# Kernel optimization log

Measured on AMD Instinct MI355X. Metric: run time of the kernel, lower is better.

Reference implementation:

```python
import jax, jax.numpy as jnp
import numpy as np

N_SRC = 50000   # e.g. users
N_DST = 50000   # e.g. items
N = N_SRC + N_DST
E = 1_600_000   # edges (avg degree ~16)
D = 64          # in_size == out_size


def _xavier(key, shape):
    # xavier_uniform for Linear(weight shape [out, in])
    fan_out, fan_in = shape
    limit = jnp.sqrt(6.0 / (fan_in + fan_out)).astype(jnp.float32)
    return jax.random.uniform(key, shape, jnp.float32, -limit, limit)


def setup_inputs() -> dict:
    key = jax.random.key(0)
    ks = jax.random.split(key, 8)
    return {
        "src_embedding": jax.random.normal(ks[0], (N_SRC, D), jnp.float32),
        "dst_embedding": jax.random.normal(ks[1], (N_DST, D), jnp.float32),
        "norm": jax.random.uniform(ks[2], (E, 1), jnp.float32),
        "W1": _xavier(ks[3], (D, D)),
        "b1": jnp.zeros((D,), jnp.float32),
        "W2": _xavier(ks[4], (D, D)),
        "b2": jnp.zeros((D,), jnp.float32),
        "edges_src": jax.random.randint(ks[5], (E,), 0, N, dtype=jnp.int32),
        "edges_dst": jax.random.randint(ks[6], (E,), 0, N, dtype=jnp.int32),
    }


def reference(src_embedding, dst_embedding, norm, W1, b1, W2, b2,
              edges_src, edges_dst):
    # concat user/item node tables: [N, D]
    x = jnp.concatenate([src_embedding, dst_embedding], axis=0)
    xs = x[edges_src]                      # [E, D] gather (edge source nodes)
    xd = x[edges_dst]                      # [E, D] gather (edge dest nodes)
    # msgs = W1(x_src) + W2(x_src * x_dst), per edge
    msgs = (jnp.einsum('ed,od->eo', xs, W1) + b1
            + jnp.einsum('ed,od->eo', xs * xd, W2) + b2)   # [E, D]
    msgs = norm * msgs                     # per-edge scalar normalization
    # copy_e + sum: scatter-sum messages onto destination nodes
    h = jax.ops.segment_sum(msgs, edges_dst, num_segments=N)  # [N, D]
    # LeakyReLU(0.2); dropout is identity in eval / p=0
    return jnp.where(h > 0, h, 0.2 * h)
```

## Files before the change

### kernel.cpp

```cpp
#include <hip/hip_runtime.h>
#include <hip/hip_bf16.h>


#define CHUNK 4096
#define NBMAX 1024
#define BCAP  2304

typedef __attribute__((ext_vector_type(8))) short short8v;
typedef __attribute__((ext_vector_type(4))) float f32x4;
union U4S8 { uint4 u; short8v s; };

__device__ __forceinline__ unsigned int f2bf(float f) {
    unsigned int u = __float_as_uint(f);
    u += 0x7fffu + ((u >> 16) & 1u);
    return u >> 16;
}
__device__ __forceinline__ unsigned int pkbf(float lo, float hi) {
    return (f2bf(hi) << 16) | f2bf(lo);
}

__global__ __launch_bounds__(256) void prep_init_kernel(
    const float* __restrict__ srcEmb, const float* __restrict__ dstEmb,
    unsigned int* __restrict__ xbf, int* __restrict__ gcur,
    int Ntot, int n_src, int NB)
{
    int i = blockIdx.x * 256 + threadIdx.x;
    if (i < NB) gcur[i] = i * BCAP;
    if (i >= Ntot * 32) return;
    int n = i >> 5, w = i & 31;
    const float* row = (n < n_src) ? srcEmb + (size_t)n * 64
                                   : dstEmb + (size_t)(n - n_src) * 64;
    xbf[i] = (f2bf(row[w + 32]) << 16) | f2bf(row[w]);
}

__global__ __launch_bounds__(1024) void part_scatter_kernel(
    const int* __restrict__ es, const int* __restrict__ ed,
    const float* __restrict__ norm, int* __restrict__ gcur,
    uint2* __restrict__ epk, int E, int NB)
{
    __shared__ int   bcnt[NBMAX];
    __shared__ int   lstart[NBMAX];
    __shared__ int   gbase[NBMAX];
    __shared__ int   sc[NBMAX];
    __shared__ uint2 sorted[CHUNK];

    int t  = threadIdx.x;
    int e0 = blockIdx.x * CHUNK;

    bcnt[t] = 0;
    __syncthreads();

    int dreg[4];
    #pragma unroll
    for (int k = 0; k < 4; ++k) {
        int e = e0 + t + k * 1024;
        dreg[k] = (e < E) ? ed[e] : -1;
        if (dreg[k] >= 0) atomicAdd(&bcnt[dreg[k] >> 7], 1);
    }
    __syncthreads();

    int c = (t < NB) ? bcnt[t] : 0;
    sc[t] = c;
    __syncthreads();
    for (int off = 1; off < NBMAX; off <<= 1) {
        int x = 0;
        if (t >= off) x = sc[t - off];
        __syncthreads();
        if (t >= off) sc[t] += x;
        __syncthreads();
    }
    int ex = sc[t] - c;
    lstart[t] = ex;
    bcnt[t]   = ex;
    if (c > 0) gbase[t] = atomicAdd(&gcur[t], c);
    __syncthreads();

    #pragma unroll
    for (int k = 0; k < 4; ++k) {
        int e = e0 + t + k * 1024;
        if (dreg[k] >= 0) {
            unsigned int q = (unsigned int)(norm[e] * 32767.f + 0.5f);
            if (q > 32767u) q = 32767u;
            int lp = atomicAdd(&bcnt[dreg[k] >> 7], 1);
            uint2 r; r.x = (unsigned int)es[e];
            r.y = ((unsigned int)dreg[k] << 15) | q;
            sorted[lp] = r;
        }
    }
    __syncthreads();

    int total = E - e0; if (total > CHUNK) total = CHUNK;
    for (int i = t; i < total; i += 1024) {
        uint2 r = sorted[i];
        int b = (int)(r.y >> 22);
        int gpos = gbase[b] + (i - lstart[b]);
        if (gpos < (b + 1) * BCAP)
            epk[gpos] = r;
    }
}

__global__ __launch_bounds__(512) void accum_fused_kernel(
    const unsigned int* __restrict__ xbf,
    const int* __restrict__ gcur, const uint2* __restrict__ epk,
    unsigned int* __restrict__ Acat, float* __restrict__ cnt, int Ntot)
{
    __shared__ uint2 srt[BCAP];
    __shared__ int   bh[128];
    __shared__ int   sc[128];
    __shared__ int   offs[129];

    int b = blockIdx.x, t = threadIdx.x;
    int base  = b * BCAP;
    int total = gcur[b] - base;
    if (total > BCAP) total = BCAP;

    if (t < 128) bh[t] = 0;
    __syncthreads();
    for (int i = t; i < total; i += 512)
        atomicAdd(&bh[(epk[base + i].y >> 15) & 127], 1);
    __syncthreads();

    int v = 0;
    if (t < 128) { v = bh[t]; sc[t] = v; }
    __syncthreads();
    for (int off = 1; off < 128; off <<= 1) {
        int x = 0;
        if (t < 128 && t >= off) x = sc[t - off];
        __syncthreads();
        if (t < 128 && t >= off) sc[t] += x;
        __syncthreads();
    }
    if (t < 128) {
        int ex = sc[t] - v;
        offs[t] = ex;
        if (t == 127) offs[128] = sc[127];
        bh[t] = ex;
    }
    __syncthreads();

    for (int i = t; i < total; i += 512) {
        uint2 r = epk[base + i];
        int pos = atomicAdd(&bh[(r.y >> 15) & 127], 1);
        srt[pos] = r;
    }
    __syncthreads();

    int lane = t & 63;
    int wv   = t >> 6;
    int sl   = lane & 7;
    int g    = lane >> 3;

    for (int li = 0; li < 16; ++li) {
        int loc = wv + li * 8;
        int n   = b * 128 + loc;
        int s0  = offs[loc];
        int s1  = offs[loc + 1];

        float ax0 = 0.f, ax1 = 0.f, ax2 = 0.f, ax3 = 0.f;
        float ay0 = 0.f, ay1 = 0.f, ay2 = 0.f, ay3 = 0.f;
        float c = 0.f;

        for (int bs2 = s0; bs2 < s1; bs2 += 64) {
            int m = s1 - bs2; if (m > 64) m = 64;
            unsigned int px = 0u, py = 0u;
            if (lane < m) { uint2 pk = srt[bs2 + lane]; px = pk.x; py = pk.y; }
            for (int k = 0; k < m; k += 16) {
                unsigned int sx0 = __shfl(px, k + g);
                unsigned int sy0 = __shfl(py, k + g);
                unsigned int sx1 = __shfl(px, k + 8 + g);
                unsigned int sy1 = __shfl(py, k + 8 + g);
                uint4 u0 = *(const uint4*)(xbf + (size_t)sx0 * 32 + 4 * sl);
                uint4 u1 = *(const uint4*)(xbf + (size_t)sx1 * 32 + 4 * sl);
                float w0 = (float)(sy0 & 0x7fffu) * (1.f / 32767.f);
                float w1 = (float)(sy1 & 0x7fffu) * (1.f / 32767.f);
                ax0 = fmaf(w0, __uint_as_float(u0.x << 16), ax0);
                ax1 = fmaf(w0, __uint_as_float(u0.y << 16), ax1);
                ax2 = fmaf(w0, __uint_as_float(u0.z << 16), ax2);
                ax3 = fmaf(w0, __uint_as_float(u0.w << 16), ax3);
                ay0 = fmaf(w0, __uint_as_float(u0.x & 0xffff0000u), ay0);
                ay1 = fmaf(w0, __uint_as_float(u0.y & 0xffff0000u), ay1);
                ay2 = fmaf(w0, __uint_as_float(u0.z & 0xffff0000u), ay2);
                ay3 = fmaf(w0, __uint_as_float(u0.w & 0xffff0000u), ay3);
                c += w0;
                ax0 = fmaf(w1, __uint_as_float(u1.x << 16), ax0);
                ax1 = fmaf(w1, __uint_as_float(u1.y << 16), ax1);
                ax2 = fmaf(w1, __uint_as_float(u1.z << 16), ax2);
                ax3 = fmaf(w1, __uint_as_float(u1.w << 16), ax3);
                ay0 = fmaf(w1, __uint_as_float(u1.x & 0xffff0000u), ay0);
                ay1 = fmaf(w1, __uint_as_float(u1.y & 0xffff0000u), ay1);
                ay2 = fmaf(w1, __uint_as_float(u1.z & 0xffff0000u), ay2);
                ay3 = fmaf(w1, __uint_as_float(u1.w & 0xffff0000u), ay3);
                c += w1;
            }
        }

        #pragma unroll
        for (int off = 8; off < 64; off <<= 1) {
            ax0 += __shfl_xor(ax0, off); ax1 += __shfl_xor(ax1, off);
            ax2 += __shfl_xor(ax2, off); ax3 += __shfl_xor(ax3, off);
            ay0 += __shfl_xor(ay0, off); ay1 += __shfl_xor(ay1, off);
            ay2 += __shfl_xor(ay2, off); ay3 += __shfl_xor(ay3, off);
            c   += __shfl_xor(c,   off);
        }

        if (g == 0 && n < Ntot) {
            uint4 xv = *(const uint4*)(xbf + (size_t)n * 32 + 4 * sl);
            float xl0 = __uint_as_float(xv.x << 16);
            float xl1 = __uint_as_float(xv.y << 16);
            float xl2 = __uint_as_float(xv.z << 16);
            float xl3 = __uint_as_float(xv.w << 16);
            float xh0 = __uint_as_float(xv.x & 0xffff0000u);
            float xh1 = __uint_as_float(xv.y & 0xffff0000u);
            float xh2 = __uint_as_float(xv.z & 0xffff0000u);
            float xh3 = __uint_as_float(xv.w & 0xffff0000u);

            uint4 w0;
            w0.x = pkbf(ax0, ax1);
            w0.y = pkbf(ax2, ax3);
            w0.z = pkbf(ay0, ay1);
            w0.w = pkbf(ay2, ay3);
            uint4 w1;
            w1.x = pkbf(ax0 * xl0, ax1 * xl1);
            w1.y = pkbf(ax2 * xl2, ax3 * xl3);
            w1.z = pkbf(ay0 * xh0, ay1 * xh1);
            w1.w = pkbf(ay2 * xh2, ay3 * xh3);
            *(uint4*)(Acat + (size_t)n * 64 + 4 * sl)      = w0;
            *(uint4*)(Acat + (size_t)n * 64 + 32 + 4 * sl) = w1;
            if (sl == 0) cnt[n] = c;
        }
    }
}

__global__ __launch_bounds__(256) void node_gemm_kernel(
    const unsigned int* __restrict__ Acat, const float* __restrict__ cnt,
    const float* __restrict__ W1, const float* __restrict__ b1,
    const float* __restrict__ W2, const float* __restrict__ b2,
    float* __restrict__ out, int Ntot)
{
    __shared__ unsigned int wlds[64 * 68];

    int t     = threadIdx.x;
    int lane  = t & 63;
    int wv    = t >> 6;
    int base  = blockIdx.x * 64;
    int row16 = lane & 15;
    int q     = lane >> 4;

    int arow = base + wv * 16 + row16;
    if (arow >= Ntot) arow = Ntot - 1;
    const uint4* ap = (const uint4*)(Acat + (size_t)arow * 64);
    uint4 af[4];
    #pragma unroll
    for (int s = 0; s < 4; ++s) af[s] = ap[s * 4 + q];

    for (int i = t; i < 64 * 64; i += 256) {
        int o = i >> 6, j = i & 63;
        int jj = j & 31, sl = jj >> 2, tt = jj & 3;
        int d0 = 4 * sl + ((tt & 1) << 1) + ((tt & 2) ? 32 : 0);
        const float* wsrc = (j < 32) ? W1 : W2;
        wlds[o * 68 + j] = pkbf(wsrc[o * 64 + d0], wsrc[o * 64 + d0 + 1]);
    }

    float cload[4];
    #pragma unroll
    for (int r = 0; r < 4; ++r) {
        int grow = base + wv * 16 + q * 4 + r;
        cload[r] = cnt[grow < Ntot ? grow : (Ntot - 1)];
    }
    f32x4 acc[4];
    #pragma unroll
    for (int j = 0; j < 4; ++j) {
        int col = j * 16 + row16;
        float bs = b1[col] + b2[col];
        #pragma unroll
        for (int r = 0; r < 4; ++r) acc[j][r] = cload[r] * bs;
    }
    __syncthreads();

    #pragma unroll
    for (int s = 0; s < 4; ++s) {
        U4S8 a; a.u = af[s];
        #pragma unroll
        for (int j = 0; j < 4; ++j) {
            int o = j * 16 + row16;
            U4S8 bb; bb.u = *(const uint4*)(wlds + o * 68 + s * 16 + q * 4);
            acc[j] = __builtin_amdgcn_mfma_f32_16x16x32_bf16(
                a.s, bb.s, acc[j], 0, 0, 0);
        }
    }

    #pragma unroll
    for (int r = 0; r < 4; ++r) {
        int grow = base + wv * 16 + q * 4 + r;
        if (grow < Ntot) {
            #pragma unroll
            for (int j = 0; j < 4; ++j) {
                float a = acc[j][r];
                out[(size_t)grow * 64 + j * 16 + row16] = (a > 0.f) ? a : 0.2f * a;
            }
        }
    }
}

extern "C" void kernel_launch(void* const* d_in, const int* in_sizes, int n_in,
                              void* d_out, int out_size, void* d_ws, size_t ws_size,
                              hipStream_t stream) {
    const float* srcEmb = (const float*)d_in[0];
    const float* dstEmb = (const float*)d_in[1];
    const float* norm   = (const float*)d_in[2];
    const float* W1     = (const float*)d_in[3];
    const float* b1     = (const float*)d_in[4];
    const float* W2     = (const float*)d_in[5];
    const float* b2     = (const float*)d_in[6];
    const int*   es     = (const int*)d_in[7];
    const int*   ed     = (const int*)d_in[8];

    const int n_src = in_sizes[0] / 64;
    const int n_dst = in_sizes[1] / 64;
    const int Ntot  = n_src + n_dst;
    const int E     = in_sizes[7];
    const int NB    = (Ntot + 127) >> 7;

    float* cnt      = (float*)d_ws;
    int*   gcur     = (int*)(cnt + Ntot);
    size_t off4     = (size_t)Ntot + NB;
    off4 = (off4 + 3) & ~(size_t)3;
    uint2* epk      = (uint2*)((float*)d_ws + off4);
    unsigned int* xbf = (unsigned int*)(epk + (size_t)NB * BCAP);
    unsigned int* Acat = (unsigned int*)d_out;

    prep_init_kernel<<<(Ntot * 32 + 255) / 256, 256, 0, stream>>>(
        srcEmb, dstEmb, xbf, gcur, Ntot, n_src, NB);

    part_scatter_kernel<<<(E + CHUNK - 1) / CHUNK, 1024, 0, stream>>>(
        es, ed, norm, gcur, epk, E, NB);

    accum_fused_kernel<<<NB, 512, 0, stream>>>(
        xbf, gcur, epk, Acat, cnt, Ntot);

    node_gemm_kernel<<<(Ntot + 63) / 64, 256, 0, stream>>>(
        Acat, cnt, W1, b1, W2, b2, (float*)d_out, Ntot);
}
```

Baseline: 199.4 us.

## Split accumulation blocks into two half-bucket blocks with wave-level prefix scan

```diff
diff --git a/kernel.cpp b/kernel.cpp
--- a/kernel.cpp
+++ b/kernel.cpp
@@ -5,6 +5,7 @@
 #define CHUNK 4096
 #define NBMAX 1024
 #define BCAP  2304
+#define SCAP  1280
 
 typedef __attribute__((ext_vector_type(8))) short short8v;
 typedef __attribute__((ext_vector_type(4))) float f32x4;
@@ -99,49 +100,56 @@
     }
 }
 
-__global__ __launch_bounds__(512) void accum_fused_kernel(
+__global__ __launch_bounds__(256) void accum_fused_kernel(
     const unsigned int* __restrict__ xbf,
     const int* __restrict__ gcur, const uint2* __restrict__ epk,
     unsigned int* __restrict__ Acat, float* __restrict__ cnt, int Ntot)
 {
-    __shared__ uint2 srt[BCAP];
-    __shared__ int   bh[128];
-    __shared__ int   sc[128];
-    __shared__ int   offs[129];
-
-    int b = blockIdx.x, t = threadIdx.x;
-    int base  = b * BCAP;
-    int total = gcur[b] - base;
+    __shared__ uint2 srt[SCAP];
+    __shared__ int   bh[64];
+    __shared__ int   offs[65];
+
+    int blk = blockIdx.x;
+    int b   = blk >> 1, h = blk & 1;
+    int t   = threadIdx.x;
+    int base    = b * BCAP;
+    int total   = gcur[b] - base;
     if (total > BCAP) total = BCAP;
-
-    if (t < 128) bh[t] = 0;
-    __syncthreads();
-    for (int i = t; i < total; i += 512)
-        atomicAdd(&bh[(epk[base + i].y >> 15) & 127], 1);
-    __syncthreads();
-
-    int v = 0;
-    if (t < 128) { v = bh[t]; sc[t] = v; }
-    __syncthreads();
-    for (int off = 1; off < 128; off <<= 1) {
-        int x = 0;
-        if (t < 128 && t >= off) x = sc[t - off];
-        __syncthreads();
-        if (t < 128 && t >= off) sc[t] += x;
-        __syncthreads();
-    }
-    if (t < 128) {
-        int ex = sc[t] - v;
+    int locbase = h << 6;
+
+    if (t < 64) bh[t] = 0;
+    __syncthreads();
+    for (int i = t; i < total; i += 256) {
+        int loc = (int)((epk[base + i].y >> 15) & 127);
+        if ((loc >> 6) == h) atomicAdd(&bh[loc & 63], 1);
+    }
+    __syncthreads();
+
+    if (t < 64) {
+        int c = bh[t];
+        int p = c;
+        #pragma unroll
+        for (int off = 1; off < 64; off <<= 1) {
+            int x = __shfl_up(p, off);
+            if (t >= off) p += x;
+        }
+        int ex = p - c;
+        if (ex > SCAP) ex = SCAP;
+        int en = p;
+        if (en > SCAP) en = SCAP;
         offs[t] = ex;
-        if (t == 127) offs[128] = sc[127];
+        if (t == 63) offs[64] = en;
         bh[t] = ex;
     }
     __syncthreads();
 
-    for (int i = t; i < total; i += 512) {
+    for (int i = t; i < total; i += 256) {
         uint2 r = epk[base + i];
-        int pos = atomicAdd(&bh[(r.y >> 15) & 127], 1);
-        srt[pos] = r;
+        int loc = (int)((r.y >> 15) & 127);
+        if ((loc >> 6) == h) {
+            int pos = atomicAdd(&bh[loc & 63], 1);
+            if (pos < SCAP) srt[pos] = r;
+        }
     }
     __syncthreads();
 
@@ -151,10 +159,10 @@
     int g    = lane >> 3;
 
     for (int li = 0; li < 16; ++li) {
-        int loc = wv + li * 8;
-        int n   = b * 128 + loc;
-        int s0  = offs[loc];
-        int s1  = offs[loc + 1];
+        int l64 = wv + (li << 2);
+        int n   = b * 128 + locbase + l64;
+        int s0  = offs[l64];
+        int s1  = offs[l64 + 1];
 
         float ax0 = 0.f, ax1 = 0.f, ax2 = 0.f, ax3 = 0.f;
         float ay0 = 0.f, ay1 = 0.f, ay2 = 0.f, ay3 = 0.f;
@@ -335,7 +343,7 @@
     part_scatter_kernel<<<(E + CHUNK - 1) / CHUNK, 1024, 0, stream>>>(
         es, ed, norm, gcur, epk, E, NB);
 
-    accum_fused_kernel<<<NB, 512, 0, stream>>>(
+    accum_fused_kernel<<<NB * 2, 256, 0, stream>>>(
         xbf, gcur, epk, Acat, cnt, Ntot);
 
     node_gemm_kernel<<<(Ntot + 63) / 64, 256, 0, stream>>>(
```

Measured after the change: 193.1 us. 3.1% less time.
